# Kernel optimization log

Hardware: AMD Instinct MI355X
Metric: run time of the kernel (lower is better)

Reference implementation:

```python
import jax, jax.numpy as jnp
import numpy as np
from jax import lax

EPS = 1e-12  # torch F.normalize eps


def _unfold3(x):
    # x: [B,C,H,W] -> [B, C*9, H*W]; matches torch F.unfold(k=3, stride=1, pad=1)
    # channel ordering (c, kh, kw), i.e. index = c*9 + kh*3 + kw
    B, C, H, W = x.shape
    xp = jnp.pad(x, ((0, 0), (0, 0), (1, 1), (1, 1)))
    pats = jnp.stack([xp[:, :, i:i + H, j:j + W] for i in range(3) for j in range(3)], axis=2)  # [B,C,9,H,W]
    return pats.reshape(B, C * 9, H * W)


def _fold3(u, H, W):
    # inverse of _unfold3 with overlap-add (torch F.fold, k=3, stride=1, pad=1)
    B, CK, L = u.shape
    C = CK // 9
    u = u.reshape(B, C, 3, 3, H, W)
    canvas = jnp.zeros((B, C, H + 2, W + 2), u.dtype)
    for i in range(3):
        for j in range(3):
            canvas = canvas.at[:, :, i:i + H, j:j + W].add(u[:, :, i, j])
    return canvas[:, :, 1:H + 1, 1:W + 1]


def setup_inputs() -> dict:
    key = jax.random.key(0)
    k1, k2, k3, k4, k5, k6 = jax.random.split(key, 6)
    B, C, H, W = 4, 64, 64, 64
    lr = jax.random.normal(k1, (B, C, H, W), dtype=jnp.float32)
    ref = jax.random.normal(k2, (B, C, H, W), dtype=jnp.float32)
    # fusion: Conv2d(2C, C, 1) then depthwise Conv2d(C, C, 3, groups=C), both with bias
    w1 = jax.random.normal(k3, (C, 2 * C, 1, 1), dtype=jnp.float32) * 0.05
    b1 = jax.random.normal(k4, (C,), dtype=jnp.float32) * 0.05
    wd = jax.random.normal(k5, (C, 1, 3, 3), dtype=jnp.float32) * 0.05
    bd = jax.random.normal(k6, (C,), dtype=jnp.float32) * 0.05
    return {"lr": lr, "ref": ref, "w1": w1, "b1": b1, "wd": wd, "bd": bd}


def reference(lr, ref, w1, b1, wd, bd):
    B, C, H, W = ref.shape
    ref_u = _unfold3(ref)          # [B, 9C, L]
    lr_u = _unfold3(lr)            # [B, 9C, L]
    ref_t = ref_u.transpose(0, 2, 1)  # [B, L, 9C]
    ref_n = ref_t / jnp.maximum(jnp.linalg.norm(ref_t, axis=2, keepdims=True), EPS)
    lr_n = lr_u / jnp.maximum(jnp.linalg.norm(lr_u, axis=1, keepdims=True), EPS)
    R = jnp.einsum('bld,bdm->blm', ref_n, lr_n)  # [B, L, L] cosine correlation
    arg = jnp.argmax(R, axis=1)                  # [B, L] best ref patch per lr position
    T_u = jnp.take_along_axis(ref_u, jnp.broadcast_to(arg[:, None, :], ref_u.shape), axis=2)
    T = _fold3(T_u, H, W)                        # [B, C, H, W]
    x = jnp.concatenate([lr, T], axis=1)         # [B, 2C, H, W]
    dn = ('NCHW', 'OIHW', 'NCHW')
    y = lax.conv_general_dilated(x, w1, (1, 1), 'VALID', dimension_numbers=dn) + b1[None, :, None, None]
    y = lax.conv_general_dilated(y, wd, (1, 1), ((1, 1), (1, 1)), dimension_numbers=dn,
                                 feature_group_count=C) + bd[None, :, None, None]
    return jax.nn.relu(y)
```

## Files before the change

kernel.cpp:

```cpp
#include <hip/hip_runtime.h>
#include <cstdint>
#include <cstddef>


#define BATCH 4
#define CCH 64
#define LPIX 4096
typedef unsigned long long u64;
typedef float f4 __attribute__((ext_vector_type(4)));

__device__ __forceinline__ u64 packKey(float v, int idx) {
    unsigned int bits = __float_as_uint(v);
    unsigned int m = (bits & 0x80000000u) ? ~bits : (bits | 0x80000000u);
    return ((u64)m << 32) | (unsigned int)(~(unsigned int)idx);
}

__global__ __launch_bounds__(256) void prep_kernel(const float* __restrict__ ref,
                                                   float* __restrict__ refT,
                                                   float* __restrict__ ssq) {
    __shared__ float s[64 * 65];
    __shared__ float part[256];
    int pt = blockIdx.x, b = blockIdx.y, tid = threadIdx.x;
    const float* rb = ref + ((size_t)b * CCH) * LPIX + pt * 64;
    for (int k = 0; k < 16; ++k) {
        int n = tid + 256 * k;
        int c = n >> 6, p = n & 63;
        s[c * 65 + p] = rb[(size_t)c * LPIX + p];
    }
    __syncthreads();
    {
        int p = tid & 63, g = tid >> 6;
        float acc = 0.f;
        for (int c = g * 16; c < g * 16 + 16; ++c) { float v = s[c * 65 + p]; acc += v * v; }
        part[g * 64 + p] = acc;
    }
    __syncthreads();
    if (tid < 64) {
        float v = part[tid] + part[64 + tid] + part[128 + tid] + part[192 + tid];
        ssq[b * LPIX + pt * 64 + tid] = v;
    }
    float* tb = refT + ((size_t)b * LPIX + pt * 64) * 64;
    for (int k = 0; k < 16; ++k) {
        int n = tid + 256 * k;
        int p = n >> 6, c = n & 63;
        tb[n] = s[c * 65 + p];
    }
}

__global__ __launch_bounds__(256) void invnorm_kernel(const float* __restrict__ ssq,
                                                      float* __restrict__ inv) {
    int t = blockIdx.x * 256 + threadIdx.x;
    int b = t >> 12, p = t & 4095;
    int y = p >> 6, x = p & 63;
    const float* sb = ssq + b * LPIX;
    float n2 = 0.f;
    for (int i = -1; i <= 1; ++i)
        for (int j = -1; j <= 1; ++j) {
            int yy = y + i, xx = x + j;
            if (yy >= 0 && yy < 64 && xx >= 0 && xx < 64) n2 += sb[yy * 64 + xx];
        }
    inv[t] = 1.0f / fmaxf(sqrtf(n2), 1e-12f);
}

__global__ __launch_bounds__(256, 2) void gemmE_kernel(const float* __restrict__ ref,
                                                       const float* __restrict__ lr,
                                                       float* __restrict__ E) {
    __shared__ __align__(16) float As[2 * 4096];
    __shared__ __align__(16) float Bs[2 * 4096];
    int bx = blockIdx.x, by = blockIdx.y, b = blockIdx.z, tid = threadIdx.x;
    const float* Ab = ref + (size_t)b * CCH * LPIX;
    const float* Bb = lr + (size_t)b * CCH * LPIX;
#pragma unroll
    for (int kk = 0; kk < 8; ++kk) {
        int n = tid + 256 * kk;
        int h = n >> 10, c = (n >> 4) & 63, q = n & 15;
        *(float4*)&As[h * 4096 + c * 64 + 4 * q] =
            *(const float4*)&Ab[(size_t)c * LPIX + (2 * by + h) * 64 + 4 * q];
        *(float4*)&Bs[h * 4096 + c * 64 + 4 * q] =
            *(const float4*)&Bb[(size_t)c * LPIX + (2 * bx + h) * 64 + 4 * q];
    }
    __syncthreads();
    int w = tid >> 6, lane = tid & 63, rg = lane >> 3, cg = lane & 7;
    const float* Ap = As + (w >> 1) * 4096 + rg * 8;
    const float* Bp = Bs + (w & 1) * 4096 + cg * 8;
    float acc[8][8] = {};
#pragma unroll 4
    for (int k = 0; k < 64; ++k) {
        float4 a0 = *(const float4*)(Ap + k * 64);
        float4 a1 = *(const float4*)(Ap + k * 64 + 4);
        float4 b0 = *(const float4*)(Bp + k * 64);
        float4 b1 = *(const float4*)(Bp + k * 64 + 4);
        float av[8] = {a0.x, a0.y, a0.z, a0.w, a1.x, a1.y, a1.z, a1.w};
        float bv[8] = {b0.x, b0.y, b0.z, b0.w, b1.x, b1.y, b1.z, b1.w};
#pragma unroll
        for (int i = 0; i < 8; ++i)
#pragma unroll
            for (int j = 0; j < 8; ++j) acc[i][j] = fmaf(av[i], bv[j], acc[i][j]);
    }
    float up[7], lf[7], dn[8], rt[8], um, dpc;
#pragma unroll
    for (int t = 0; t < 7; ++t) up[t] = __shfl(acc[7][t], lane - 8, 64);
    um = __shfl(acc[7][7], lane - 9, 64);
#pragma unroll
    for (int t = 0; t < 7; ++t) lf[t] = __shfl(acc[t][7], lane - 1, 64);
#pragma unroll
    for (int t = 1; t < 8; ++t) dn[t] = __shfl(acc[0][t], lane + 8, 64);
    dpc = __shfl(acc[0][0], lane + 9, 64);
#pragma unroll
    for (int t = 1; t < 8; ++t) rt[t] = __shfl(acc[t][0], lane + 1, 64);

    int r1 = 2 * by + (w >> 1), r2 = 2 * bx + (w & 1);
    float* Et = E + ((size_t)b << 24) + ((size_t)((r1 << 6) + r2) << 12) + (rg * 8) * 64 + cg * 8;
    bool rgt = rg > 0, rlt = rg < 7, cgt = cg > 0, clt = cg < 7;
#pragma unroll
    for (int i = 0; i < 8; ++i) {
        float e[8];
#pragma unroll
        for (int j = 0; j < 8; ++j) {
            float dm, dpv;
            if (i >= 1) dm = (j >= 1) ? acc[i - 1][j - 1] : (cgt ? lf[i - 1] : 0.f);
            else        dm = rgt ? ((j >= 1) ? up[j - 1] : (cgt ? um : 0.f)) : 0.f;
            if (i <= 6) dpv = (j <= 6) ? acc[i + 1][j + 1] : (clt ? rt[i + 1] : 0.f);
            else        dpv = rlt ? ((j <= 6) ? dn[j + 1] : (clt ? dpc : 0.f)) : 0.f;
            e[j] = dm + acc[i][j] + dpv;
        }
        f4 o0 = {e[0], e[1], e[2], e[3]};
        f4 o1 = {e[4], e[5], e[6], e[7]};
        __builtin_nontemporal_store(o0, (f4*)(Et + i * 64));
        __builtin_nontemporal_store(o1, (f4*)(Et + i * 64 + 4));
    }
}

__global__ __launch_bounds__(256) void band_kernel(const float* __restrict__ E,
                                                   const float* __restrict__ inv,
                                                   u64* __restrict__ packed) {
    __shared__ u64 red[16 * 65];
    int b = blockIdx.z;
    int k = (int)blockIdx.y - 63;
    int t_lo = k < 0 ? -k : 0;
    int t_hi = 64 - (k > 0 ? k : 0);
    int y0 = t_lo + (int)blockIdx.x * 16;
    if (y0 >= t_hi) return;
    int y1 = y0 + 16 < t_hi ? y0 + 16 : t_hi;
    const float* Ebase = E + ((size_t)b << 24);
    const float* invb = inv + b * LPIX;
    u64* pkb = packed + (size_t)b * LPIX;
    int tid = threadIdx.x;
    int c4 = tid & 15, s = tid >> 4;

    float4 Ea[4], Eb[4], Ec[4];
    auto LOADT = [&](float4* T, int t) {
        if (t >= t_lo && t < t_hi) {
            const float4* tp = (const float4*)(Ebase + ((size_t)(((t + k) << 6) + t) << 12));
#pragma unroll
            for (int i = 0; i < 4; ++i) T[i] = tp[tid + 256 * i];
        } else {
#pragma unroll
            for (int i = 0; i < 4; ++i) T[i] = make_float4(0.f, 0.f, 0.f, 0.f);
        }
    };
    LOADT(Ea, y0 - 1); LOADT(Eb, y0); LOADT(Ec, y0 + 1);

    for (int y = y0; y < y1; ++y) {
        int yprow = (y + k) << 6;
        u64 kc0 = 0, kc1 = 0, kc2 = 0, kc3 = 0;
#pragma unroll
        for (int i = 0; i < 4; ++i) {
            int xr = s + 16 * i;
            float iv = invb[yprow + xr];
            int idx = yprow + xr;
            float vx = (Ea[i].x + Eb[i].x + Ec[i].x) * iv;
            float vy = (Ea[i].y + Eb[i].y + Ec[i].y) * iv;
            float vz = (Ea[i].z + Eb[i].z + Ec[i].z) * iv;
            float vw = (Ea[i].w + Eb[i].w + Ec[i].w) * iv;
            u64 t0 = packKey(vx, idx); kc0 = kc0 > t0 ? kc0 : t0;
            u64 t1 = packKey(vy, idx); kc1 = kc1 > t1 ? kc1 : t1;
            u64 t2 = packKey(vz, idx); kc2 = kc2 > t2 ? kc2 : t2;
            u64 t3 = packKey(vw, idx); kc3 = kc3 > t3 ? kc3 : t3;
        }
        red[s * 65 + 4 * c4 + 0] = kc0;
        red[s * 65 + 4 * c4 + 1] = kc1;
        red[s * 65 + 4 * c4 + 2] = kc2;
        red[s * 65 + 4 * c4 + 3] = kc3;
        __syncthreads();
        if (tid < 64) {
            u64 m = red[tid];
#pragma unroll
            for (int ss = 1; ss < 16; ++ss) {
                u64 v = red[ss * 65 + tid];
                m = m > v ? m : v;
            }
            atomicMax(&pkb[(y << 6) + tid], m);
        }
        __syncthreads();
        if (y + 1 < y1) {
            float4 En[4];
            LOADT(En, y + 2);
#pragma unroll
            for (int i = 0; i < 4; ++i) { Ea[i] = Eb[i]; Eb[i] = Ec[i]; Ec[i] = En[i]; }
        }
    }
}

__global__ __launch_bounds__(256) void gather_kernel(const u64* __restrict__ packed,
                                                     const float* __restrict__ refT,
                                                     float* __restrict__ Tt) {
    int b = blockIdx.y;
    int wave = threadIdx.x >> 6, lane = threadIdx.x & 63;
    int p = blockIdx.x * 4 + wave;
    int py = p >> 6, px = p & 63;
    const u64* pk = packed + (size_t)b * LPIX;
    const float* rT = refT + (size_t)b * LPIX * 64;
    float acc = 0.f;
#pragma unroll
    for (int i = 0; i < 3; ++i)
#pragma unroll
        for (int j = 0; j < 3; ++j) {
            int qy = py + 1 - i, qx = px + 1 - j;
            if ((unsigned)qy >= 64u || (unsigned)qx >= 64u) continue;
            int aidx = (int)(~(unsigned int)pk[qy * 64 + qx]);
            int ry = (aidx >> 6) + i - 1, rx = (aidx & 63) + j - 1;
            if ((unsigned)ry >= 64u || (unsigned)rx >= 64u) continue;
            acc += rT[(size_t)(ry * 64 + rx) * 64 + lane];
        }
    Tt[((size_t)b * LPIX + p) * 64 + lane] = acc;
}

#define XST 36
__global__ __launch_bounds__(256) void conv1_kernel(const float* __restrict__ lr,
                                                    const float* __restrict__ Tt,
                                                    const float* __restrict__ w1,
                                                    const float* __restrict__ b1,
                                                    float* __restrict__ z) {
    __shared__ __align__(16) float xs[128 * XST];
    __shared__ __align__(16) float wsm[64 * 128];
    int pt = blockIdx.x, b = blockIdx.y, tid = threadIdx.x;
    for (int k = 0; k < 8; ++k) {
        int n = tid + 256 * k;
        *(float4*)&wsm[4 * n] = *(const float4*)&w1[4 * n];
    }
    const float* lrb = lr + (size_t)b * CCH * LPIX + pt * 32;
    for (int k = 0; k < 2; ++k) {
        int n = tid + 256 * k;
        int c = n >> 3, q = n & 7;
        *(float4*)&xs[c * XST + 4 * q] = *(const float4*)&lrb[(size_t)c * LPIX + 4 * q];
    }
    const float* Tb = Tt + ((size_t)b * LPIX + pt * 32) * 64;
    for (int k = 0; k < 2; ++k) {
        int n = tid + 256 * k;
        int p = n >> 4, cq = n & 15;
        float4 v = *(const float4*)&Tb[p * 64 + 4 * cq];
        xs[(64 + 4 * cq + 0) * XST + p] = v.x;
        xs[(64 + 4 * cq + 1) * XST + p] = v.y;
        xs[(64 + 4 * cq + 2) * XST + p] = v.z;
        xs[(64 + 4 * cq + 3) * XST + p] = v.w;
    }
    __syncthreads();
    int p = tid & 31, g = tid >> 5;
    float acc[8];
#pragma unroll
    for (int t = 0; t < 8; ++t) acc[t] = b1[g * 8 + t];
    for (int c = 0; c < 128; ++c) {
        float xv = xs[c * XST + p];
#pragma unroll
        for (int t = 0; t < 8; ++t) acc[t] = fmaf(wsm[(g * 8 + t) * 128 + c], xv, acc[t]);
    }
    float* zb = z + (size_t)b * CCH * LPIX + pt * 32;
#pragma unroll
    for (int t = 0; t < 8; ++t) zb[(size_t)(g * 8 + t) * LPIX + p] = acc[t];
}

__global__ __launch_bounds__(256) void dw_kernel(const float* __restrict__ z,
                                                 const float* __restrict__ wd,
                                                 const float* __restrict__ bd,
                                                 float* __restrict__ out) {
    __shared__ __align__(16) float zs[4096];
    int c = blockIdx.x, b = blockIdx.y, tid = threadIdx.x;
    const float* zb = z + ((size_t)b * CCH + c) * LPIX;
    for (int k = 0; k < 4; ++k) {
        int n = tid + 256 * k;
        *(float4*)&zs[4 * n] = *(const float4*)&zb[4 * n];
    }
    __syncthreads();
    float w[9];
#pragma unroll
    for (int t = 0; t < 9; ++t) w[t] = wd[c * 9 + t];
    float bias = bd[c];
    float* ob = out + ((size_t)b * CCH + c) * LPIX;
    for (int s = 0; s < 16; ++s) {
        int p = tid + 256 * s;
        int y = p >> 6, x = p & 63;
        float acc = bias;
#pragma unroll
        for (int i = 0; i < 3; ++i) {
            int yy = y + i - 1;
            if ((unsigned)yy >= 64u) continue;
#pragma unroll
            for (int j = 0; j < 3; ++j) {
                int xx = x + j - 1;
                if ((unsigned)xx >= 64u) continue;
                acc = fmaf(zs[yy * 64 + xx], w[i * 3 + j], acc);
            }
        }
        ob[p] = fmaxf(acc, 0.f);
    }
}

extern "C" void kernel_launch(void* const* d_in, const int* in_sizes, int n_in,
                              void* d_out, int out_size, void* d_ws, size_t ws_size,
                              hipStream_t stream) {
    const float* lr  = (const float*)d_in[0];
    const float* ref = (const float*)d_in[1];
    const float* w1  = (const float*)d_in[2];
    const float* b1  = (const float*)d_in[3];
    const float* wd  = (const float*)d_in[4];
    const float* bd  = (const float*)d_in[5];
    float* out = (float*)d_out;

    float* ws = (float*)d_ws;
    float* refT = ws;
    float* ssq  = refT + (size_t)1048576;
    float* inv  = ssq + 16384;
    u64* packed = (u64*)(inv + 16384);
    float* Tt = (float*)(packed + 16384);
    float* z  = Tt + (size_t)1048576;
    float* E  = z + (size_t)1048576;

    const size_t base = 12845056ull;
    const size_t per  = 67108864ull;
    int NB = (ws_size >= base + 4 * per) ? 4 : (ws_size >= base + 2 * per) ? 2 : 1;

    hipMemsetAsync(packed, 0, (size_t)BATCH * LPIX * sizeof(u64), stream);
    prep_kernel<<<dim3(64, BATCH), 256, 0, stream>>>(ref, refT, ssq);
    invnorm_kernel<<<dim3(64), 256, 0, stream>>>(ssq, inv);
    for (int b0 = 0; b0 < BATCH; b0 += NB) {
        gemmE_kernel<<<dim3(32, 32, NB), 256, 0, stream>>>(
            ref + (size_t)b0 * CCH * LPIX, lr + (size_t)b0 * CCH * LPIX, E);
        band_kernel<<<dim3(4, 127, NB), 256, 0, stream>>>(
            E, inv + (size_t)b0 * LPIX, packed + (size_t)b0 * LPIX);
    }
    gather_kernel<<<dim3(1024, BATCH), 256, 0, stream>>>(packed, refT, Tt);
    conv1_kernel<<<dim3(128, BATCH), 256, 0, stream>>>(lr, Tt, w1, b1, z);
    dw_kernel<<<dim3(64, BATCH), 256, 0, stream>>>(z, wd, bd, out);
}
```

Measured before the change: 312.3 us.

## Split E batches into pairs, add cached stores, shuffle-reduce band argmax with deeper prefetch

The E buffer is now computed for two batches at a time instead of up to four. The second pair is written with ordinary cached stores, so the band kernel may find it in the large last-level cache. The band kernel swaps its shared-memory reduction and two block barriers for wave-level shuffle-xor max reductions. It also remaps thread-to-element indexing and prefetches two rows ahead instead of one. The cost is an extra launch pair when the workspace is large, and higher register pressure from the added prefetch buffers.

Result: slower. 471.9 us (+51.1%).

```diff
diff --git a/kernel.cpp b/kernel.cpp
--- a/kernel.cpp
+++ b/kernel.cpp
@@ -62,6 +62,7 @@
     inv[t] = 1.0f / fmaxf(sqrtf(n2), 1e-12f);
 }
 
+template <bool NT>
 __global__ __launch_bounds__(256, 2) void gemmE_kernel(const float* __restrict__ ref,
                                                        const float* __restrict__ lr,
                                                        float* __restrict__ E) {
@@ -124,17 +125,21 @@
             else        dpv = rlt ? ((j <= 6) ? dn[j + 1] : (clt ? dpc : 0.f)) : 0.f;
             e[j] = dm + acc[i][j] + dpv;
         }
-        f4 o0 = {e[0], e[1], e[2], e[3]};
-        f4 o1 = {e[4], e[5], e[6], e[7]};
-        __builtin_nontemporal_store(o0, (f4*)(Et + i * 64));
-        __builtin_nontemporal_store(o1, (f4*)(Et + i * 64 + 4));
+        if (NT) {
+            f4 o0 = {e[0], e[1], e[2], e[3]};
+            f4 o1 = {e[4], e[5], e[6], e[7]};
+            __builtin_nontemporal_store(o0, (f4*)(Et + i * 64));
+            __builtin_nontemporal_store(o1, (f4*)(Et + i * 64 + 4));
+        } else {
+            *(float4*)(Et + i * 64)     = make_float4(e[0], e[1], e[2], e[3]);
+            *(float4*)(Et + i * 64 + 4) = make_float4(e[4], e[5], e[6], e[7]);
+        }
     }
 }
 
 __global__ __launch_bounds__(256) void band_kernel(const float* __restrict__ E,
                                                    const float* __restrict__ inv,
                                                    u64* __restrict__ packed) {
-    __shared__ u64 red[16 * 65];
     int b = blockIdx.z;
     int k = (int)blockIdx.y - 63;
     int t_lo = k < 0 ? -k : 0;
@@ -146,58 +151,58 @@
     const float* invb = inv + b * LPIX;
     u64* pkb = packed + (size_t)b * LPIX;
     int tid = threadIdx.x;
-    int c4 = tid & 15, s = tid >> 4;
-
-    float4 Ea[4], Eb[4], Ec[4];
+    int w = tid >> 6, l = tid & 63;
+    int lg = l >> 4, xq = l & 15;
+
+    float4 Ea[4], Eb[4], Ec[4], P0[4], P1[4];
     auto LOADT = [&](float4* T, int t) {
         if (t >= t_lo && t < t_hi) {
             const float4* tp = (const float4*)(Ebase + ((size_t)(((t + k) << 6) + t) << 12));
 #pragma unroll
-            for (int i = 0; i < 4; ++i) T[i] = tp[tid + 256 * i];
+            for (int i = 0; i < 4; ++i) T[i] = tp[(w << 8) + (i << 6) + l];
         } else {
 #pragma unroll
             for (int i = 0; i < 4; ++i) T[i] = make_float4(0.f, 0.f, 0.f, 0.f);
         }
     };
     LOADT(Ea, y0 - 1); LOADT(Eb, y0); LOADT(Ec, y0 + 1);
+    LOADT(P0, y0 + 2); LOADT(P1, y0 + 3);
 
     for (int y = y0; y < y1; ++y) {
         int yprow = (y + k) << 6;
-        u64 kc0 = 0, kc1 = 0, kc2 = 0, kc3 = 0;
+        u64 key[4] = {0, 0, 0, 0};
 #pragma unroll
         for (int i = 0; i < 4; ++i) {
-            int xr = s + 16 * i;
-            float iv = invb[yprow + xr];
-            int idx = yprow + xr;
+            int xp = (w << 4) + (i << 2) + lg;
+            float iv = invb[yprow + xp];
+            int idx = yprow + xp;
             float vx = (Ea[i].x + Eb[i].x + Ec[i].x) * iv;
             float vy = (Ea[i].y + Eb[i].y + Ec[i].y) * iv;
             float vz = (Ea[i].z + Eb[i].z + Ec[i].z) * iv;
             float vw = (Ea[i].w + Eb[i].w + Ec[i].w) * iv;
-            u64 t0 = packKey(vx, idx); kc0 = kc0 > t0 ? kc0 : t0;
-            u64 t1 = packKey(vy, idx); kc1 = kc1 > t1 ? kc1 : t1;
-            u64 t2 = packKey(vz, idx); kc2 = kc2 > t2 ? kc2 : t2;
-            u64 t3 = packKey(vw, idx); kc3 = kc3 > t3 ? kc3 : t3;
-        }
-        red[s * 65 + 4 * c4 + 0] = kc0;
-        red[s * 65 + 4 * c4 + 1] = kc1;
-        red[s * 65 + 4 * c4 + 2] = kc2;
-        red[s * 65 + 4 * c4 + 3] = kc3;
-        __syncthreads();
-        if (tid < 64) {
-            u64 m = red[tid];
-#pragma unroll
-            for (int ss = 1; ss < 16; ++ss) {
-                u64 v = red[ss * 65 + tid];
-                m = m > v ? m : v;
+            u64 t0 = packKey(vx, idx); key[0] = key[0] > t0 ? key[0] : t0;
+            u64 t1 = packKey(vy, idx); key[1] = key[1] > t1 ? key[1] : t1;
+            u64 t2 = packKey(vz, idx); key[2] = key[2] > t2 ? key[2] : t2;
+            u64 t3 = packKey(vw, idx); key[3] = key[3] > t3 ? key[3] : t3;
+        }
+#pragma unroll
+        for (int d = 16; d <= 32; d <<= 1)
+#pragma unroll
+            for (int j = 0; j < 4; ++j) {
+                u64 o = __shfl_xor(key[j], d, 64);
+                key[j] = key[j] > o ? key[j] : o;
             }
-            atomicMax(&pkb[(y << 6) + tid], m);
-        }
-        __syncthreads();
+        if (lg == 0) {
+            int cb = (y << 6) + (xq << 2);
+#pragma unroll
+            for (int j = 0; j < 4; ++j) atomicMax(&pkb[cb + j], key[j]);
+        }
         if (y + 1 < y1) {
-            float4 En[4];
-            LOADT(En, y + 2);
-#pragma unroll
-            for (int i = 0; i < 4; ++i) { Ea[i] = Eb[i]; Eb[i] = Ec[i]; Ec[i] = En[i]; }
+#pragma unroll
+            for (int i = 0; i < 4; ++i) {
+                Ea[i] = Eb[i]; Eb[i] = Ec[i]; Ec[i] = P0[i]; P0[i] = P1[i];
+            }
+            LOADT(P1, y + 4);
         }
     }
 }
@@ -328,16 +333,25 @@
 
     const size_t base = 12845056ull;
     const size_t per  = 67108864ull;
-    int NB = (ws_size >= base + 4 * per) ? 4 : (ws_size >= base + 2 * per) ? 2 : 1;
+    int NB = (ws_size >= base + 2 * per) ? 2 : 1;
 
     hipMemsetAsync(packed, 0, (size_t)BATCH * LPIX * sizeof(u64), stream);
     prep_kernel<<<dim3(64, BATCH), 256, 0, stream>>>(ref, refT, ssq);
     invnorm_kernel<<<dim3(64), 256, 0, stream>>>(ssq, inv);
-    for (int b0 = 0; b0 < BATCH; b0 += NB) {
-        gemmE_kernel<<<dim3(32, 32, NB), 256, 0, stream>>>(
-            ref + (size_t)b0 * CCH * LPIX, lr + (size_t)b0 * CCH * LPIX, E);
-        band_kernel<<<dim3(4, 127, NB), 256, 0, stream>>>(
-            E, inv + (size_t)b0 * LPIX, packed + (size_t)b0 * LPIX);
+    if (NB == 2) {
+        gemmE_kernel<true><<<dim3(32, 32, 2), 256, 0, stream>>>(ref, lr, E);
+        band_kernel<<<dim3(4, 127, 2), 256, 0, stream>>>(E, inv, packed);
+        gemmE_kernel<false><<<dim3(32, 32, 2), 256, 0, stream>>>(
+            ref + (size_t)2 * CCH * LPIX, lr + (size_t)2 * CCH * LPIX, E);
+        band_kernel<<<dim3(4, 127, 2), 256, 0, stream>>>(
+            E, inv + (size_t)2 * LPIX, packed + (size_t)2 * LPIX);
+    } else {
+        for (int b0 = 0; b0 < BATCH; ++b0) {
+            gemmE_kernel<false><<<dim3(32, 32, 1), 256, 0, stream>>>(
+                ref + (size_t)b0 * CCH * LPIX, lr + (size_t)b0 * CCH * LPIX, E);
+            band_kernel<<<dim3(4, 127, 1), 256, 0, stream>>>(
+                E, inv + (size_t)b0 * LPIX, packed + (size_t)b0 * LPIX);
+        }
     }
     gather_kernel<<<dim3(1024, BATCH), 256, 0, stream>>>(packed, refT, Tt);
     conv1_kernel<<<dim3(128, BATCH), 256, 0, stream>>>(lr, Tt, w1, b1, z);
```
